# Kernel optimization log

Hardware: AMD Instinct MI355X
Metric: run time of the kernel (lower is better)

The kernel has to match this reference:

```python
import jax, jax.numpy as jnp
import numpy as np

N_HEADS, D_MODEL, D_HEAD = 16, 1024, 64
INIT_RANGE = 0.02
BATCH, SEQ = 4, 2048


def setup_inputs() -> dict:
    key = jax.random.key(0)
    k0, k1, k2, k3, k4 = jax.random.split(key, 5)
    resid = jax.random.normal(k0, (BATCH, SEQ, D_MODEL), dtype=jnp.float32)
    w_q = INIT_RANGE * jax.random.normal(k1, (N_HEADS, D_MODEL, D_HEAD), dtype=jnp.float32)
    w_k = INIT_RANGE * jax.random.normal(k2, (N_HEADS, D_MODEL, D_HEAD), dtype=jnp.float32)
    w_v = INIT_RANGE * jax.random.normal(k3, (N_HEADS, D_MODEL, D_HEAD), dtype=jnp.float32)
    w_o = INIT_RANGE * jax.random.normal(k4, (N_HEADS, D_HEAD, D_MODEL), dtype=jnp.float32)
    return {"resid": resid, "w_q": w_q, "w_k": w_k, "w_v": w_v, "w_o": w_o}


def reference(resid, w_q, w_k, w_v, w_o):
    # resid: [b, s, m]; w_q/k/v: [h, m, d]; w_o: [h, d, m]
    qs = jnp.einsum('bsm,hmd->bhsd', resid, w_q)
    ks = jnp.einsum('bsm,hmd->bhsd', resid, w_k)
    vs = jnp.einsum('bsm,hmd->bhsd', resid, w_v)
    attn = jnp.einsum('bhqd,bhkd->bhqk', qs, ks)  # full O(n^2) scores
    s = attn.shape[-1]
    causal = jnp.tril(jnp.ones((s, s), dtype=bool))  # True = keep
    attn = jnp.where(causal, attn, -jnp.inf)
    attn = jax.nn.softmax(attn / jnp.sqrt(jnp.float32(D_HEAD)), axis=-1)
    z = jnp.einsum('bhqk,bhkd->bhqd', attn, vs)
    out = jnp.einsum('bhsd,hdm->bsm', z, w_o)
    return out
```

## Files before the change

kernel.cpp:

```cpp
#include <hip/hip_runtime.h>


typedef __attribute__((ext_vector_type(8))) short short8;
typedef __attribute__((ext_vector_type(4))) float f32x4;
typedef __attribute__((ext_vector_type(16))) float f32x16;

#define GLDS16(g, l) __builtin_amdgcn_global_load_lds(                        \
    (const __attribute__((address_space(1))) unsigned int*)(g),               \
    (__attribute__((address_space(3))) unsigned int*)(l), 16, 0, 0)

#define VM0 asm volatile("s_waitcnt vmcnt(0)" ::: "memory")

static __device__ __forceinline__ unsigned short f2b(float f) {
  union { float f; unsigned u; } c; c.f = f;
  unsigned r = c.u + 0x7fffu + ((c.u >> 16) & 1u);
  return (unsigned short)(r >> 16);
}

static __device__ __forceinline__ int swzc(int row, int c) {
  return (c & ~31) | ((((c >> 3) & 3) ^ ((row >> 1) & 3)) << 3) | (c & 7);
}

__global__ void k_cast(const float* __restrict__ x, unsigned short* __restrict__ o, int n4) {
  int i = blockIdx.x * blockDim.x + threadIdx.x;
  if (i >= n4) return;
  float4 v = reinterpret_cast<const float4*>(x)[i];
  ushort4 u;
  u.x = f2b(v.x); u.y = f2b(v.y); u.z = f2b(v.z); u.w = f2b(v.w);
  const int flat = i * 4;
  const int row = flat >> 10, c = flat & 1023;
  *reinterpret_cast<ushort4*>(&o[row * 1024 + swzc(row, c)]) = u;
}

__global__ void k_trans_qkv(const float* __restrict__ wq, const float* __restrict__ wk,
                            const float* __restrict__ wv, unsigned short* __restrict__ o) {
  __shared__ float t[64][65];
  int blk = blockIdx.x;
  int mt = blk & 15;
  int h = (blk >> 4) & 15;
  int which = blk >> 8;
  const float* w = which == 0 ? wq : (which == 1 ? wk : wv);
  int tid = threadIdx.x;
  int m0 = mt * 64;
  #pragma unroll
  for (int rep = 0; rep < 16; ++rep) {
    int idx = rep * 256 + tid;
    int r = idx >> 6, c = idx & 63;
    t[r][c] = w[(h * 1024 + m0 + r) * 64 + c];
  }
  __syncthreads();
  #pragma unroll
  for (int rep = 0; rep < 16; ++rep) {
    int idx = rep * 256 + tid;
    int dr = idx >> 6, mc = idx & 63;
    const int row = which * 1024 + h * 64 + dr;
    o[row * 1024 + swzc(dr, m0 + mc)] = f2b(t[mc][dr]);
  }
}

__global__ void k_trans_wo(const float* __restrict__ wo, unsigned short* __restrict__ o) {
  __shared__ float t[64][65];
  int blk = blockIdx.x;
  int mt = blk & 15, kt = blk >> 4;
  int tid = threadIdx.x;
  int k0 = kt * 64, m0 = mt * 64;
  #pragma unroll
  for (int rep = 0; rep < 16; ++rep) {
    int idx = rep * 256 + tid;
    int r = idx >> 6, c = idx & 63;
    t[r][c] = wo[(k0 + r) * 1024 + m0 + c];
  }
  __syncthreads();
  #pragma unroll
  for (int rep = 0; rep < 16; ++rep) {
    int idx = rep * 256 + tid;
    int r = idx >> 6, c = idx & 63;
    o[(m0 + r) * 1024 + swzc(r, k0 + c)] = f2b(t[c][r]);
  }
}

__global__ __launch_bounds__(256) void k_gemm_qkv(const unsigned short* __restrict__ A,
                                                  const unsigned short* __restrict__ Bt,
                                                  unsigned short* __restrict__ Qb,
                                                  unsigned short* __restrict__ Kc,
                                                  unsigned short* __restrict__ Vc) {
  __shared__ unsigned short As[2][128 * 32];
  __shared__ unsigned short Bs[2][128 * 32];
  const int bm = blockIdx.x, bn = blockIdx.y;
  const int tid = threadIdx.x;
  const int lane = tid & 63, wid = tid >> 6;
  const int wr = wid >> 1, wc = wid & 1;
  const int fr = lane & 15, fq = lane >> 4;

  f32x4 acc[4][4];
  #pragma unroll
  for (int i = 0; i < 4; ++i)
    #pragma unroll
    for (int n = 0; n < 4; ++n) acc[i][n] = f32x4{0.f, 0.f, 0.f, 0.f};

  const int arow = tid >> 2, acol = (tid & 3) * 8;
  const int lds0 = tid * 8, lds1 = (tid + 256) * 8;
  const unsigned short* aG0 = A + (bm * 128 + arow) * 1024 + acol;
  const unsigned short* aG1 = A + (bm * 128 + arow + 64) * 1024 + acol;
  const unsigned short* bG0 = Bt + (bn * 128 + arow) * 1024 + acol;
  const unsigned short* bG1 = Bt + (bn * 128 + arow + 64) * 1024 + acol;

  const int rowA = (wr * 64 + fr) * 32;
  const int rowB = (wc * 64 + fr) * 32;
  const int slot = ((fq ^ ((fr >> 1) & 3)) << 3);

  for (int k0 = 0; k0 < 1024; k0 += 64) {
    __syncthreads();
    GLDS16(aG0 + k0,      As[0] + lds0);
    GLDS16(aG1 + k0,      As[0] + lds1);
    GLDS16(aG0 + k0 + 32, As[1] + lds0);
    GLDS16(aG1 + k0 + 32, As[1] + lds1);
    GLDS16(bG0 + k0,      Bs[0] + lds0);
    GLDS16(bG1 + k0,      Bs[0] + lds1);
    GLDS16(bG0 + k0 + 32, Bs[1] + lds0);
    GLDS16(bG1 + k0 + 32, Bs[1] + lds1);
    VM0;
    __syncthreads();
    #pragma unroll
    for (int p = 0; p < 2; ++p) {
      short8 a[4], b[4];
      #pragma unroll
      for (int i = 0; i < 4; ++i)
        a[i] = *reinterpret_cast<const short8*>(As[p] + rowA + i * 512 + slot);
      #pragma unroll
      for (int n = 0; n < 4; ++n)
        b[n] = *reinterpret_cast<const short8*>(Bs[p] + rowB + n * 512 + slot);
      #pragma unroll
      for (int i = 0; i < 4; ++i)
        #pragma unroll
        for (int n = 0; n < 4; ++n)
          acc[i][n] = __builtin_amdgcn_mfma_f32_16x16x32_bf16(a[i], b[n], acc[i][n], 0, 0, 0);
    }
  }

  const float CS = 0.125f * 1.44269504088896340736f;
  const int colb = bn * 128 + wc * 64 + fr;
  const int rowb = bm * 128 + wr * 64 + fq * 4;
  #pragma unroll
  for (int n = 0; n < 4; ++n) {
    const int col = colb + n * 16;
    const int which = col >> 10, rc = col & 1023;
    const int h = rc >> 6, d = rc & 63;
    #pragma unroll
    for (int i = 0; i < 4; ++i) {
      const int row = rowb + i * 16;
      const int b_ = row >> 11, s = row & 2047;
      const int bh = b_ * 16 + h;
      if (which == 2) {
        const int c = s >> 5, kk = s & 31;
        const int r = d >> 1;
        const int sl = (((d & 1) * 4 + (kk >> 3)) ^ (r & 7));
        ushort4 v;
        v.x = f2b(acc[i][n][0]); v.y = f2b(acc[i][n][1]);
        v.z = f2b(acc[i][n][2]); v.w = f2b(acc[i][n][3]);
        *reinterpret_cast<ushort4*>(
            &Vc[((size_t)(bh * 64 + c)) * 2048 + r * 64 + sl * 8 + (kk & 7)]) = v;
      } else if (which == 1) {
        #pragma unroll
        for (int j = 0; j < 4; ++j) {
          const int ss = s + j;
          const int c = ss >> 5, r = ss & 31;
          const int dsw = (((d >> 3) ^ (r & 7)) << 3) | (d & 7);
          Kc[(((size_t)(bh * 64 + c)) * 32 + r) * 64 + dsw] = f2b(acc[i][n][j]);
        }
      } else {
        unsigned short* dst = Qb + ((size_t)bh * 2048 + s) * 64 + d;
        #pragma unroll
        for (int j = 0; j < 4; ++j) dst[j * 64] = f2b(acc[i][n][j] * CS);
      }
    }
  }
}


static __device__ __forceinline__ f32x16 mfma32(short8 a, short8 b, f32x16 c) {
  return __builtin_amdgcn_mfma_f32_32x32x16_bf16(a, b, c, 0, 0, 0);
}

template<bool MASKED>
static __device__ __forceinline__ void compute_chunk(
    const unsigned short* __restrict__ Kl, const unsigned short* __restrict__ Vl,
    int q, int hi,
    const short8& Qf0, const short8& Qf1, const short8& Qf2, const short8& Qf3,
    f32x16& accA, f32x16& accB, float& lsum) {
  const int qs = q & 7;
  const short8 kf0 = *reinterpret_cast<const short8*>(Kl + q * 64 + (((0 + hi) ^ qs) << 3));
  const short8 kf1 = *reinterpret_cast<const short8*>(Kl + q * 64 + (((2 + hi) ^ qs) << 3));
  const short8 kf2 = *reinterpret_cast<const short8*>(Kl + q * 64 + (((4 + hi) ^ qs) << 3));
  const short8 kf3 = *reinterpret_cast<const short8*>(Kl + q * 64 + (((6 + hi) ^ qs) << 3));
  const int vr = q >> 1, vs = (q & 1) * 4, vw = vr & 7;
  const short8 v00 = *reinterpret_cast<const short8*>(Vl + vr * 64 + (((vs + hi) ^ vw) << 3));
  const short8 v01 = *reinterpret_cast<const short8*>(Vl + vr * 64 + (((vs + 2 + hi) ^ vw) << 3));
  const short8 v10 = *reinterpret_cast<const short8*>(Vl + (vr + 16) * 64 + (((vs + hi) ^ vw) << 3));
  const short8 v11 = *reinterpret_cast<const short8*>(Vl + (vr + 16) * 64 + (((vs + 2 + hi) ^ vw) << 3));

  f32x16 s = {0.f,0.f,0.f,0.f,0.f,0.f,0.f,0.f,0.f,0.f,0.f,0.f,0.f,0.f,0.f,0.f};
  s = mfma32(kf0, Qf0, s);
  s = mfma32(kf1, Qf1, s);
  s = mfma32(kf2, Qf2, s);
  s = mfma32(kf3, Qf3, s);

  float p[16];
  #pragma unroll
  for (int r = 0; r < 16; ++r) {
    if (MASKED) {
      const int kr = (r & 3) + 8 * (r >> 2) + 4 * hi;
      p[r] = (kr <= q) ? __builtin_amdgcn_exp2f(s[r]) : 0.f;
    } else {
      p[r] = __builtin_amdgcn_exp2f(s[r]);
    }
  }
  float t0 = (p[0] + p[1]) + (p[2] + p[3]);
  float t1 = (p[4] + p[5]) + (p[6] + p[7]);
  float t2 = (p[8] + p[9]) + (p[10] + p[11]);
  float t3 = (p[12] + p[13]) + (p[14] + p[15]);
  lsum += (t0 + t1) + (t2 + t3);

  unsigned W[8], X[8];
  #pragma unroll
  for (int i = 0; i < 8; ++i)
    asm("v_cvt_pk_bf16_f32 %0, %1, %2" : "=v"(W[i]) : "v"(p[2 * i]), "v"(p[2 * i + 1]));
  #pragma unroll
  for (int i = 0; i < 8; ++i) X[i] = __shfl_xor(W[i], 32);

  union { unsigned u[4]; short8 v; } fa0, fa1;
  fa0.u[0] = hi ? X[2] : W[0];
  fa0.u[1] = hi ? X[3] : W[1];
  fa0.u[2] = hi ? W[2] : X[0];
  fa0.u[3] = hi ? W[3] : X[1];
  fa1.u[0] = hi ? X[6] : W[4];
  fa1.u[1] = hi ? X[7] : W[5];
  fa1.u[2] = hi ? W[6] : X[4];
  fa1.u[3] = hi ? W[7] : X[5];

  accA = mfma32(fa0.v, v00, accA);
  accA = mfma32(fa1.v, v01, accA);
  accB = mfma32(fa0.v, v10, accB);
  accB = mfma32(fa1.v, v11, accB);
}

static __device__ __forceinline__ void store_tile(unsigned short* __restrict__ Zb,
    int b_, int h, int q0, int q, int hi,
    const f32x16& a0, const f32x16& a1, float lsum) {
  const float lt = lsum + __shfl_xor(lsum, 32);
  const float rl = 1.f / lt;
  #pragma unroll
  for (int r = 0; r < 16; ++r) {
    const int qr = (r & 3) + 8 * (r >> 2) + 4 * hi;
    const float rlr = __shfl(rl, qr);
    const int row = b_ * 2048 + q0 + qr;
    const int sl = (((q >> 3) ^ ((qr >> 1) & 3)) << 3) + (q & 7);
    unsigned short* dst = Zb + (size_t)row * 1024 + h * 64;
    dst[sl]      = f2b(a0[r] * rlr);
    dst[32 + sl] = f2b(a1[r] * rlr);
  }
}

__global__ __launch_bounds__(256, 2) void k_attn(const unsigned short* __restrict__ Qb,
                                                 const unsigned short* __restrict__ Kc,
                                                 const unsigned short* __restrict__ Vc,
                                                 unsigned short* __restrict__ Zb) {
  __shared__ __align__(16) unsigned short Kbuf[3][2048];
  __shared__ __align__(16) unsigned short Vbuf[3][2048];
  const int tid = threadIdx.x;
  const int lane = tid & 63, w = tid >> 6;
  const int q = lane & 31, hi = lane >> 5;
  const int bid = blockIdx.x;
  const int g = bid & 7;
  const int sdec = bid >> 3;
  const int par = sdec & 1;
  const int jj = sdec >> 1;
  const int bh = g * 8 + (jj & 7);
  const int x = jj >> 3;
  const int P1 = par ? (7 - x) : x;
  const int q0A = 128 * P1 + 32 * w;
  const int q0B = 128 * (15 - P1) + 32 * w;
  const int cmaxA = 4 * P1 + w;
  const int cmaxB = 4 * (15 - P1) + w;
  const int C = 4 * (15 - P1) + 4;
  const int b_ = bh >> 4, h = bh & 15;

  const unsigned short* Qbh = Qb + (size_t)bh * 2048 * 64;
  const unsigned short* Kch = Kc + (size_t)bh * 64 * 2048;
  const unsigned short* Vch = Vc + (size_t)bh * 64 * 2048;

  const unsigned short* QpA = Qbh + (size_t)(q0A + q) * 64 + hi * 8;
  const short8 QA0 = *reinterpret_cast<const short8*>(QpA);
  const short8 QA1 = *reinterpret_cast<const short8*>(QpA + 16);
  const short8 QA2 = *reinterpret_cast<const short8*>(QpA + 32);
  const short8 QA3 = *reinterpret_cast<const short8*>(QpA + 48);
  const unsigned short* QpB = Qbh + (size_t)(q0B + q) * 64 + hi * 8;
  const short8 QB0 = *reinterpret_cast<const short8*>(QpB);
  const short8 QB1 = *reinterpret_cast<const short8*>(QpB + 16);
  const short8 QB2 = *reinterpret_cast<const short8*>(QpB + 32);
  const short8 QB3 = *reinterpret_cast<const short8*>(QpB + 48);

  const f32x16 zero = {0.f,0.f,0.f,0.f,0.f,0.f,0.f,0.f,0.f,0.f,0.f,0.f,0.f,0.f,0.f,0.f};
  f32x16 aA0 = zero, aA1 = zero, aB0 = zero, aB1 = zero;
  float lA = 0.f, lB = 0.f;

  GLDS16(Kch + tid * 8,        &Kbuf[0][tid * 8]);
  GLDS16(Vch + tid * 8,        &Vbuf[0][tid * 8]);
  GLDS16(Kch + 2048 + tid * 8, &Kbuf[1][tid * 8]);
  GLDS16(Vch + 2048 + tid * 8, &Vbuf[1][tid * 8]);

  int ci = 0, si = 2;
  for (int c = 0; c < C; ++c) {
    if (c == C - 1) { VM0; }
    else            { asm volatile("s_waitcnt vmcnt(2)" ::: "memory"); }
    __syncthreads();
    if (c + 2 < C) {
      GLDS16(Kch + (size_t)(c + 2) * 2048 + tid * 8, &Kbuf[si][tid * 8]);
      GLDS16(Vch + (size_t)(c + 2) * 2048 + tid * 8, &Vbuf[si][tid * 8]);
    }
    if (c <= cmaxA) {
      if (c == cmaxA)
        compute_chunk<true >(Kbuf[ci], Vbuf[ci], q, hi, QA0, QA1, QA2, QA3, aA0, aA1, lA);
      else
        compute_chunk<false>(Kbuf[ci], Vbuf[ci], q, hi, QA0, QA1, QA2, QA3, aA0, aA1, lA);
    }
    if (c <= cmaxB) {
      if (c == cmaxB)
        compute_chunk<true >(Kbuf[ci], Vbuf[ci], q, hi, QB0, QB1, QB2, QB3, aB0, aB1, lB);
      else
        compute_chunk<false>(Kbuf[ci], Vbuf[ci], q, hi, QB0, QB1, QB2, QB3, aB0, aB1, lB);
    }
    ci = (ci + 1 == 3) ? 0 : ci + 1;
    si = (si + 1 == 3) ? 0 : si + 1;
  }
  store_tile(Zb, b_, h, q0A, q, hi, aA0, aA1, lA);
  store_tile(Zb, b_, h, q0B, q, hi, aB0, aB1, lB);
}

__global__ __launch_bounds__(256) void k_gemm_out(const unsigned short* __restrict__ A,
                                                  const unsigned short* __restrict__ Bt,
                                                  float* __restrict__ Out) {
  __shared__ unsigned short As[2][128 * 32];
  __shared__ unsigned short Bs[2][128 * 32];
  const int bm = blockIdx.x, bn = blockIdx.y;
  const int tid = threadIdx.x;
  const int lane = tid & 63, wid = tid >> 6;
  const int wr = wid >> 1, wc = wid & 1;
  const int fr = lane & 15, fq = lane >> 4;

  f32x4 acc[4][4];
  #pragma unroll
  for (int i = 0; i < 4; ++i)
    #pragma unroll
    for (int n = 0; n < 4; ++n) acc[i][n] = f32x4{0.f, 0.f, 0.f, 0.f};

  const int arow = tid >> 2, acol = (tid & 3) * 8;
  const int lds0 = tid * 8, lds1 = (tid + 256) * 8;
  const unsigned short* aG0 = A + (bm * 128 + arow) * 1024 + acol;
  const unsigned short* aG1 = A + (bm * 128 + arow + 64) * 1024 + acol;
  const unsigned short* bG0 = Bt + (bn * 128 + arow) * 1024 + acol;
  const unsigned short* bG1 = Bt + (bn * 128 + arow + 64) * 1024 + acol;

  const int rowA = (wr * 64 + fr) * 32;
  const int rowB = (wc * 64 + fr) * 32;
  const int slot = ((fq ^ ((fr >> 1) & 3)) << 3);

  for (int k0 = 0; k0 < 1024; k0 += 64) {
    __syncthreads();
    GLDS16(aG0 + k0,      As[0] + lds0);
    GLDS16(aG1 + k0,      As[0] + lds1);
    GLDS16(aG0 + k0 + 32, As[1] + lds0);
    GLDS16(aG1 + k0 + 32, As[1] + lds1);
    GLDS16(bG0 + k0,      Bs[0] + lds0);
    GLDS16(bG1 + k0,      Bs[0] + lds1);
    GLDS16(bG0 + k0 + 32, Bs[1] + lds0);
    GLDS16(bG1 + k0 + 32, Bs[1] + lds1);
    VM0;
    __syncthreads();
    #pragma unroll
    for (int p = 0; p < 2; ++p) {
      short8 a[4], b[4];
      #pragma unroll
      for (int i = 0; i < 4; ++i)
        a[i] = *reinterpret_cast<const short8*>(As[p] + rowA + i * 512 + slot);
      #pragma unroll
      for (int n = 0; n < 4; ++n)
        b[n] = *reinterpret_cast<const short8*>(Bs[p] + rowB + n * 512 + slot);
      #pragma unroll
      for (int i = 0; i < 4; ++i)
        #pragma unroll
        for (int n = 0; n < 4; ++n)
          acc[i][n] = __builtin_amdgcn_mfma_f32_16x16x32_bf16(a[i], b[n], acc[i][n], 0, 0, 0);
    }
  }

  const int colb = bn * 128 + wc * 64 + fr;
  const int rowb = bm * 128 + wr * 64 + fq * 4;
  #pragma unroll
  for (int n = 0; n < 4; ++n) {
    const int col = colb + n * 16;
    #pragma unroll
    for (int i = 0; i < 4; ++i) {
      const int row = rowb + i * 16;
      #pragma unroll
      for (int j = 0; j < 4; ++j) Out[(size_t)(row + j) * 1024 + col] = acc[i][n][j];
    }
  }
}

extern "C" void kernel_launch(void* const* d_in, const int* in_sizes, int n_in,
                              void* d_out, int out_size, void* d_ws, size_t ws_size,
                              hipStream_t stream) {
  const float* resid = (const float*)d_in[0];
  const float* w_q = (const float*)d_in[1];
  const float* w_k = (const float*)d_in[2];
  const float* w_v = (const float*)d_in[3];
  const float* w_o = (const float*)d_in[4];
  float* out = (float*)d_out;

  char* ws = (char*)d_ws;
  const size_t MB = 1u << 20;
  unsigned short* Xb = (unsigned short*)(ws);
  unsigned short* W3 = (unsigned short*)(ws + 16 * MB);
  unsigned short* Wo = (unsigned short*)(ws + 22 * MB);
  unsigned short* Qb = (unsigned short*)(ws + 24 * MB);
  unsigned short* Kc = (unsigned short*)(ws + 40 * MB);
  unsigned short* Vc = (unsigned short*)(ws + 56 * MB);
  unsigned short* Zb = Xb;

  hipLaunchKernelGGL(k_cast, dim3(8192), dim3(256), 0, stream, resid, Xb, 8192 * 1024 / 4);
  hipLaunchKernelGGL(k_trans_qkv, dim3(768), dim3(256), 0, stream, w_q, w_k, w_v, W3);
  hipLaunchKernelGGL(k_trans_wo, dim3(256), dim3(256), 0, stream, w_o, Wo);
  hipLaunchKernelGGL(k_gemm_qkv, dim3(64, 24), dim3(256), 0, stream, Xb, W3, Qb, Kc, Vc);
  hipLaunchKernelGGL(k_attn, dim3(512), dim3(256), 0, stream, Qb, Kc, Vc, Zb);
  hipLaunchKernelGGL(k_gemm_out, dim3(64, 8), dim3(256), 0, stream, Zb, Wo, out);
}
```

Baseline: 165.0 us.

## Stage K/V chunk pairs per barrier, share fragments, raise MFMA priority

The attention loop now stages two 32-key K/V chunks per pipeline step into a 3-deep ring of paired buffers. This halves the number of __syncthreads barriers and waits per row. K/V fragments are loaded from LDS once and reused for both query tiles A and B, where before they were read twice. MFMA sequences are wrapped in s_setprio to favour matrix issue across waves. LDS use doubles to 48KB per block, which may limit occupancy at two blocks per CU.

```diff
diff --git a/kernel.cpp b/kernel.cpp
--- a/kernel.cpp
+++ b/kernel.cpp
@@ -182,28 +182,36 @@
   return __builtin_amdgcn_mfma_f32_32x32x16_bf16(a, b, c, 0, 0, 0);
 }
 
+struct KVf { short8 k0, k1, k2, k3, v0, v1, v2, v3; };
+
+static __device__ __forceinline__ KVf load_frags(
+    const unsigned short* __restrict__ Kl, const unsigned short* __restrict__ Vl,
+    int q, int hi) {
+  KVf f;
+  const int qs = q & 7;
+  f.k0 = *reinterpret_cast<const short8*>(Kl + q * 64 + (((0 + hi) ^ qs) << 3));
+  f.k1 = *reinterpret_cast<const short8*>(Kl + q * 64 + (((2 + hi) ^ qs) << 3));
+  f.k2 = *reinterpret_cast<const short8*>(Kl + q * 64 + (((4 + hi) ^ qs) << 3));
+  f.k3 = *reinterpret_cast<const short8*>(Kl + q * 64 + (((6 + hi) ^ qs) << 3));
+  const int vr = q >> 1, vs = (q & 1) * 4, vw = vr & 7;
+  f.v0 = *reinterpret_cast<const short8*>(Vl + vr * 64 + (((vs + hi) ^ vw) << 3));
+  f.v1 = *reinterpret_cast<const short8*>(Vl + vr * 64 + (((vs + 2 + hi) ^ vw) << 3));
+  f.v2 = *reinterpret_cast<const short8*>(Vl + (vr + 16) * 64 + (((vs + hi) ^ vw) << 3));
+  f.v3 = *reinterpret_cast<const short8*>(Vl + (vr + 16) * 64 + (((vs + 2 + hi) ^ vw) << 3));
+  return f;
+}
+
 template<bool MASKED>
-static __device__ __forceinline__ void compute_chunk(
-    const unsigned short* __restrict__ Kl, const unsigned short* __restrict__ Vl,
-    int q, int hi,
+static __device__ __forceinline__ void tile_math(const KVf& f, int q, int hi,
     const short8& Qf0, const short8& Qf1, const short8& Qf2, const short8& Qf3,
     f32x16& accA, f32x16& accB, float& lsum) {
-  const int qs = q & 7;
-  const short8 kf0 = *reinterpret_cast<const short8*>(Kl + q * 64 + (((0 + hi) ^ qs) << 3));
-  const short8 kf1 = *reinterpret_cast<const short8*>(Kl + q * 64 + (((2 + hi) ^ qs) << 3));
-  const short8 kf2 = *reinterpret_cast<const short8*>(Kl + q * 64 + (((4 + hi) ^ qs) << 3));
-  const short8 kf3 = *reinterpret_cast<const short8*>(Kl + q * 64 + (((6 + hi) ^ qs) << 3));
-  const int vr = q >> 1, vs = (q & 1) * 4, vw = vr & 7;
-  const short8 v00 = *reinterpret_cast<const short8*>(Vl + vr * 64 + (((vs + hi) ^ vw) << 3));
-  const short8 v01 = *reinterpret_cast<const short8*>(Vl + vr * 64 + (((vs + 2 + hi) ^ vw) << 3));
-  const short8 v10 = *reinterpret_cast<const short8*>(Vl + (vr + 16) * 64 + (((vs + hi) ^ vw) << 3));
-  const short8 v11 = *reinterpret_cast<const short8*>(Vl + (vr + 16) * 64 + (((vs + 2 + hi) ^ vw) << 3));
-
   f32x16 s = {0.f,0.f,0.f,0.f,0.f,0.f,0.f,0.f,0.f,0.f,0.f,0.f,0.f,0.f,0.f,0.f};
-  s = mfma32(kf0, Qf0, s);
-  s = mfma32(kf1, Qf1, s);
-  s = mfma32(kf2, Qf2, s);
-  s = mfma32(kf3, Qf3, s);
+  __builtin_amdgcn_s_setprio(1);
+  s = mfma32(f.k0, Qf0, s);
+  s = mfma32(f.k1, Qf1, s);
+  s = mfma32(f.k2, Qf2, s);
+  s = mfma32(f.k3, Qf3, s);
+  __builtin_amdgcn_s_setprio(0);
 
   float p[16];
   #pragma unroll
@@ -238,10 +246,12 @@
   fa1.u[2] = hi ? W[6] : X[4];
   fa1.u[3] = hi ? W[7] : X[5];
 
-  accA = mfma32(fa0.v, v00, accA);
-  accA = mfma32(fa1.v, v01, accA);
-  accB = mfma32(fa0.v, v10, accB);
-  accB = mfma32(fa1.v, v11, accB);
+  __builtin_amdgcn_s_setprio(1);
+  accA = mfma32(fa0.v, f.v0, accA);
+  accA = mfma32(fa1.v, f.v1, accA);
+  accB = mfma32(fa0.v, f.v2, accB);
+  accB = mfma32(fa1.v, f.v3, accB);
+  __builtin_amdgcn_s_setprio(0);
 }
 
 static __device__ __forceinline__ void store_tile(unsigned short* __restrict__ Zb,
@@ -265,8 +275,8 @@
                                                  const unsigned short* __restrict__ Kc,
                                                  const unsigned short* __restrict__ Vc,
                                                  unsigned short* __restrict__ Zb) {
-  __shared__ __align__(16) unsigned short Kbuf[3][2048];
-  __shared__ __align__(16) unsigned short Vbuf[3][2048];
+  __shared__ __align__(16) unsigned short Kbuf[3][2][2048];
+  __shared__ __align__(16) unsigned short Vbuf[3][2][2048];
   const int tid = threadIdx.x;
   const int lane = tid & 63, w = tid >> 6;
   const int q = lane & 31, hi = lane >> 5;
@@ -283,6 +293,7 @@
   const int cmaxA = 4 * P1 + w;
   const int cmaxB = 4 * (15 - P1) + w;
   const int C = 4 * (15 - P1) + 4;
+  const int R = C >> 1;
   const int b_ = bh >> 4, h = bh & 15;
 
   const unsigned short* Qbh = Qb + (size_t)bh * 2048 * 64;
@@ -304,37 +315,44 @@
   f32x16 aA0 = zero, aA1 = zero, aB0 = zero, aB1 = zero;
   float lA = 0.f, lB = 0.f;
 
-  GLDS16(Kch + tid * 8,        &Kbuf[0][tid * 8]);
-  GLDS16(Vch + tid * 8,        &Vbuf[0][tid * 8]);
-  GLDS16(Kch + 2048 + tid * 8, &Kbuf[1][tid * 8]);
-  GLDS16(Vch + 2048 + tid * 8, &Vbuf[1][tid * 8]);
+#define STAGE_PAIR(r, si)                                                     \
+    GLDS16(Kch + (size_t)(2 * (r)) * 2048 + tid * 8,     &Kbuf[si][0][tid * 8]); \
+    GLDS16(Vch + (size_t)(2 * (r)) * 2048 + tid * 8,     &Vbuf[si][0][tid * 8]); \
+    GLDS16(Kch + (size_t)(2 * (r) + 1) * 2048 + tid * 8, &Kbuf[si][1][tid * 8]); \
+    GLDS16(Vch + (size_t)(2 * (r) + 1) * 2048 + tid * 8, &Vbuf[si][1][tid * 8]);
+
+  STAGE_PAIR(0, 0);
+  STAGE_PAIR(1, 1);
 
   int ci = 0, si = 2;
-  for (int c = 0; c < C; ++c) {
-    if (c == C - 1) { VM0; }
-    else            { asm volatile("s_waitcnt vmcnt(2)" ::: "memory"); }
+  for (int r = 0; r < R; ++r) {
+    if (r == R - 1) { VM0; }
+    else            { asm volatile("s_waitcnt vmcnt(4)" ::: "memory"); }
     __syncthreads();
-    if (c + 2 < C) {
-      GLDS16(Kch + (size_t)(c + 2) * 2048 + tid * 8, &Kbuf[si][tid * 8]);
-      GLDS16(Vch + (size_t)(c + 2) * 2048 + tid * 8, &Vbuf[si][tid * 8]);
-    }
-    if (c <= cmaxA) {
-      if (c == cmaxA)
-        compute_chunk<true >(Kbuf[ci], Vbuf[ci], q, hi, QA0, QA1, QA2, QA3, aA0, aA1, lA);
-      else
-        compute_chunk<false>(Kbuf[ci], Vbuf[ci], q, hi, QA0, QA1, QA2, QA3, aA0, aA1, lA);
-    }
-    if (c <= cmaxB) {
-      if (c == cmaxB)
-        compute_chunk<true >(Kbuf[ci], Vbuf[ci], q, hi, QB0, QB1, QB2, QB3, aB0, aB1, lB);
-      else
-        compute_chunk<false>(Kbuf[ci], Vbuf[ci], q, hi, QB0, QB1, QB2, QB3, aB0, aB1, lB);
+    if (r + 2 < R) { STAGE_PAIR(r + 2, si); }
+    #pragma unroll
+    for (int half = 0; half < 2; ++half) {
+      const int c = 2 * r + half;
+      if (c <= cmaxB) {
+        const KVf f = load_frags(Kbuf[ci][half], Vbuf[ci][half], q, hi);
+        if (c <= cmaxA) {
+          if (c == cmaxA)
+            tile_math<true >(f, q, hi, QA0, QA1, QA2, QA3, aA0, aA1, lA);
+          else
+            tile_math<false>(f, q, hi, QA0, QA1, QA2, QA3, aA0, aA1, lA);
+        }
+        if (c == cmaxB)
+          tile_math<true >(f, q, hi, QB0, QB1, QB2, QB3, aB0, aB1, lB);
+        else
+          tile_math<false>(f, q, hi, QB0, QB1, QB2, QB3, aB0, aB1, lB);
+      }
     }
     ci = (ci + 1 == 3) ? 0 : ci + 1;
     si = (si + 1 == 3) ? 0 : si + 1;
   }
   store_tile(Zb, b_, h, q0A, q, hi, aA0, aA1, lA);
   store_tile(Zb, b_, h, q0B, q, hi, aB0, aB1, lB);
+#undef STAGE_PAIR
 }
 
 __global__ __launch_bounds__(256) void k_gemm_out(const unsigned short* __restrict__ A,
```

Result: faster. 161.0 us, median of 2 (-2.4%).
